# Kernel tuning notes

Hardware: AMD Instinct MI355X
Metric: run time of the kernel (lower is better)

The kernel has to match this reference:

```python
import jax, jax.numpy as jnp
import numpy as np

# Standard SMPL kinematic tree parents (kintree_table)
PARENTS = np.array([-1, 0, 0, 0, 1, 2, 3, 4, 5, 6, 7, 8, 9, 9, 9,
                    12, 13, 14, 16, 17, 18, 19, 20, 21])
NV, NJ, NB, NP = 6890, 24, 10, 207


def rodrigues(r):
    """Axis-angle [N,3] -> rotation matrices [N,3,3] (Rodrigues formula)."""
    theta = jnp.linalg.norm(r, axis=1, keepdims=True) + 1e-8  # [N,1]
    rh = r / theta                                            # [N,3]
    cos = jnp.cos(theta)[..., None]                           # [N,1,1]
    sin = jnp.sin(theta)[..., None]
    z = jnp.zeros_like(rh[:, 0])
    m = jnp.stack([z, -rh[:, 2], rh[:, 1],
                   rh[:, 2], z, -rh[:, 0],
                   -rh[:, 1], rh[:, 0], z], axis=1).reshape(-1, 3, 3)
    dot = rh[:, :, None] * rh[:, None, :]                     # outer product
    eye = jnp.eye(3, dtype=r.dtype)
    return cos * eye + (1.0 - cos) * dot + sin * m


def setup_inputs() -> dict:
    key = jax.random.key(0)
    ks = jax.random.split(key, 9)
    B = 512
    betas = jax.random.normal(ks[0], (B, NB), dtype=jnp.float32)
    thetas = jax.random.normal(ks[1], (B, NJ * 3), dtype=jnp.float32) * 0.3
    trans = jax.random.normal(ks[2], (B, 3), dtype=jnp.float32)
    scale = jnp.ones((1,), dtype=jnp.float32)
    v_template = jax.random.normal(ks[3], (NV, 3), dtype=jnp.float32)
    shapedirs = jax.random.normal(ks[4], (NV, 3, NB), dtype=jnp.float32) * 0.01
    posedirs = jax.random.normal(ks[5], (NV, 3, NP), dtype=jnp.float32) * 0.01
    Jr = jax.random.uniform(ks[6], (NJ, NV), dtype=jnp.float32)
    J_regressor = Jr / jnp.sum(Jr, axis=1, keepdims=True)
    w = jax.random.uniform(ks[7], (NV, NJ), dtype=jnp.float32)
    weights = w / jnp.sum(w, axis=1, keepdims=True)
    return {"betas": betas, "thetas": thetas, "trans": trans, "scale": scale,
            "v_template": v_template, "shapedirs": shapedirs,
            "posedirs": posedirs, "J_regressor": J_regressor,
            "weights": weights}


def reference(betas, thetas, trans, scale, v_template, shapedirs, posedirs,
              J_regressor, weights):
    B = betas.shape[0]
    dt = betas.dtype
    # Shape blend shapes: v_shaped [B, 6890, 3]
    v_shaped = jnp.einsum('bs,vcs->bvc', betas, shapedirs) + v_template
    # Rest-pose joints J(beta): [B, 24, 3]
    J = jnp.einsum('jv,bvc->bjc', J_regressor, v_shaped)
    # Local rotations from axis-angle, root scaled by `scale`
    lRs = rodrigues(thetas.reshape(-1, 3)).reshape(B, NJ, 3, 3)
    lRs = lRs.at[:, 0].multiply(scale[0])
    # Local joint offsets: root keeps J[:,0], children use J[i] - J[parent[i]]
    parents = jnp.asarray(PARENTS)
    t = J - J[:, jnp.clip(parents, 0)]
    t = t.at[:, 0].set(J[:, 0])
    # Local 4x4 transforms [B, 24, 4, 4]
    top = jnp.concatenate([lRs, t[..., None]], axis=3)          # [B,24,3,4]
    bottom = jnp.broadcast_to(jnp.array([0., 0., 0., 1.], dtype=dt),
                              (B, NJ, 1, 4))
    A = jnp.concatenate([top, bottom], axis=2)
    # Kinematic chain accumulation (fixed 24-joint tree)
    results = [A[:, 0]]
    for i in range(1, NJ):
        results.append(results[PARENTS[i]] @ A[:, i])
    stacked = jnp.stack(results, axis=1)                         # [B,24,4,4]
    # Remove rest-pose joint locations from translation column
    Jh = jnp.concatenate([J, jnp.zeros((B, NJ, 1), dtype=dt)], axis=2)
    deformed = jnp.einsum('bjxy,bjy->bjx', stacked, Jh)          # [B,24,4]
    G = stacked.at[..., 3].add(-deformed)
    # Pose blend shapes from non-root rotations
    lrotmin = (lRs[:, 1:] - jnp.eye(3, dtype=dt)).reshape(B, -1)  # [B,207]
    v_posed = v_shaped + jnp.einsum('bp,vcp->bvc', lrotmin, posedirs)
    # Linear blend skinning
    T = jnp.einsum('bjxy,vj->bvxy', G, weights)                  # [B,6890,4,4]
    vh = jnp.concatenate([v_posed, jnp.ones((B, NV, 1), dtype=dt)], axis=2)
    v = jnp.einsum('bvxy,bvy->bvx', T, vh)[:, :, :3]
    result = v + trans[:, None, :]
    joints = jnp.einsum('jv,bvc->bjc', J_regressor, result)
    return result, joints
```

## Files before the change

### kernel.cpp

```cpp
#include <hip/hip_runtime.h>

#define NVERT 6890
#define NJNT  24
#define NBETA 10
#define NPOSE 207
#define NBATCH 512
#define KPAD 224
#define MROWS 20736
#define NVC (NVERT * 3)

#define NBA 18144
#define NBW 1728
#define NJR 576

typedef __attribute__((ext_vector_type(8))) short short8;
typedef __attribute__((ext_vector_type(4))) float floatx4;

__constant__ int c_par[NJNT]   = {-1,0,0,0,1,2,3,4,5,6,7,8,9,9,9,12,13,14,16,17,18,19,20,21};
__constant__ int c_depth[NJNT] = { 0,1,1,1,2,2,2,3,3,3,4,4,4,4,4,5,5,5,6,6,7,7,8,8};

static __device__ __forceinline__ unsigned short f2bf(float x) {
  union { float f; unsigned u; } v; v.f = x;
  unsigned r = (v.u + 0x7FFFu + ((v.u >> 16) & 1u)) >> 16;
  return (unsigned short)r;
}
static __device__ __forceinline__ float bf2f(unsigned short h) {
  union { unsigned u; float f; } v; v.u = (unsigned)h << 16;
  return v.f;
}

__global__ __launch_bounds__(256) void k_prep(
    const float* __restrict__ pdir, const float* __restrict__ sd,
    const float* __restrict__ vt, const float* __restrict__ wgt,
    const float* __restrict__ Jr,
    unsigned short* __restrict__ AT, unsigned short* __restrict__ W16,
    float* __restrict__ wsJP) {
  const int bx = blockIdx.x;
  const int tid = threadIdx.x;
  if (bx < NBA) {
    const int idx = bx * 256 + tid;
    const int kk = idx & 31;
    const int row = (idx >> 5) % MROWS;
    const int kt = idx / (MROWS * 32);
    const int k = kt * 32 + kk;
    float val = 0.f;
    if (row < NVC) {
      if (k < NPOSE)            val = pdir[(size_t)row * NPOSE + k];
      else if (k < NPOSE + 10)  val = sd[(size_t)row * 10 + (k - NPOSE)];
      else if (k == NPOSE + 10) val = vt[row];
    }
    AT[idx] = f2bf(val);
  } else if (bx < NBA + NBW) {
    const int idx = (bx - NBA) * 256 + tid;
    const int v = idx >> 6, c = idx & 63, j = c & 31;
    const float w = (v < NVERT && j < 24) ? wgt[(size_t)v * 24 + j] : 0.f;
    const unsigned short hi = f2bf(w);
    W16[idx] = (c >> 5) ? f2bf(w - bf2f(hi)) : hi;
  } else {
    const int jb = bx - (NBA + NBW);
    const int jc = jb % 72, j = jc / 3, c = jc % 3;
    const int chunk = jb / 72;
    const int v0 = chunk * 864;
    const int vend = min(NVERT, v0 + 864);
    float acc[11];
    #pragma unroll
    for (int k = 0; k < 11; ++k) acc[k] = 0.f;
    for (int v = v0 + tid; v < vend; v += 256) {
      const float w = Jr[j * NVERT + v];
      acc[0] += w * vt[v * 3 + c];
      const float* s = sd + (size_t)v * 30 + c * 10;
      #pragma unroll
      for (int k = 0; k < 10; ++k) acc[1 + k] += w * s[k];
    }
    #pragma unroll
    for (int off = 32; off > 0; off >>= 1) {
      #pragma unroll
      for (int k = 0; k < 11; ++k) acc[k] += __shfl_down(acc[k], off, 64);
    }
    __shared__ float red[4][11];
    const int lane = tid & 63, wv = tid >> 6;
    if (lane == 0) {
      #pragma unroll
      for (int k = 0; k < 11; ++k) red[wv][k] = acc[k];
    }
    __syncthreads();
    if (tid == 0) {
      #pragma unroll
      for (int k = 0; k < 11; ++k)
        wsJP[(size_t)(chunk * 72 + jc) * 11 + k] =
            red[0][k] + red[1][k] + red[2][k] + red[3][k];
    }
  }
}

__global__ __launch_bounds__(256, 2) void k_chain3(
    const float* __restrict__ betas, const float* __restrict__ thetas,
    const float* __restrict__ scale, const float* __restrict__ trans,
    const float* __restrict__ wsJP,
    unsigned short* __restrict__ BT, unsigned short* __restrict__ G16) {
  __shared__ __align__(16) float sJ[792];
  __shared__ __align__(16) float sJJ[4][72];
  __shared__ __align__(16) float sM[4][288];
  __shared__ __align__(16) unsigned short sG[4][1024];
  __shared__ __align__(16) unsigned short sB[4][KPAD];

  const int tid = threadIdx.x;
  const int wv = tid >> 6, lane = tid & 63;
  const int b = blockIdx.x * 4 + wv;

  if (tid < 72) {
    #pragma unroll
    for (int k = 0; k < 11; ++k) {
      float s = 0.f;
      #pragma unroll
      for (int c8 = 0; c8 < 8; ++c8) s += wsJP[(size_t)(c8 * 72 + tid) * 11 + k];
      if (k == 0) sJ[tid] = s;
      else        sJ[72 + tid * 10 + (k - 1)] = s;
    }
  }
  #pragma unroll
  for (int r = 0; r < 4; ++r) {
    sG[wv][lane * 16 + r * 4 + 0] = 0; sG[wv][lane * 16 + r * 4 + 1] = 0;
    sG[wv][lane * 16 + r * 4 + 2] = 0; sG[wv][lane * 16 + r * 4 + 3] = 0;
  }
  __syncthreads();

  float R[9], t[3], M[12], Jx = 0.f, Jy = 0.f, Jz = 0.f;
  const int i = lane;
  if (i < NJNT) {
    #pragma unroll
    for (int c = 0; c < 3; ++c) {
      float a = sJ[i * 3 + c];
      const float* d = sJ + 72 + (i * 3 + c) * 10;
      #pragma unroll
      for (int s = 0; s < NBETA; ++s) a += d[s] * betas[b * NBETA + s];
      if (c == 0) Jx = a; else if (c == 1) Jy = a; else Jz = a;
    }
    sJJ[wv][i * 3 + 0] = Jx; sJJ[wv][i * 3 + 1] = Jy; sJJ[wv][i * 3 + 2] = Jz;
    const float rx = thetas[b * 72 + i * 3 + 0];
    const float ry = thetas[b * 72 + i * 3 + 1];
    const float rz = thetas[b * 72 + i * 3 + 2];
    const float th = sqrtf(rx * rx + ry * ry + rz * rz) + 1e-8f;
    const float inv = 1.f / th;
    const float x = rx * inv, y = ry * inv, z = rz * inv;
    const float cs = cosf(th), sn = sinf(th), omc = 1.f - cs;
    R[0] = cs + omc * x * x;     R[1] = omc * x * y - sn * z; R[2] = omc * x * z + sn * y;
    R[3] = omc * x * y + sn * z; R[4] = cs + omc * y * y;     R[5] = omc * y * z - sn * x;
    R[6] = omc * x * z - sn * y; R[7] = omc * y * z + sn * x; R[8] = cs + omc * z * z;
    if (i == 0) {
      const float sc = scale[0];
      #pragma unroll
      for (int k = 0; k < 9; ++k) R[k] *= sc;
    } else {
      #pragma unroll
      for (int k = 0; k < 9; ++k)
        sB[wv][(i - 1) * 9 + k] = f2bf(R[k] - ((k == 0 || k == 4 || k == 8) ? 1.f : 0.f));
    }
  }
  if (i == 0) {
    #pragma unroll
    for (int s = 0; s < NBETA; ++s) sB[wv][NPOSE + s] = f2bf(betas[b * NBETA + s]);
    sB[wv][NPOSE + 10] = 0x3F80;
    #pragma unroll
    for (int k = NPOSE + 11; k < KPAD; ++k) sB[wv][k] = 0;
  }
  __syncthreads();

  if (i < NJNT) {
    if (i == 0) { t[0] = Jx; t[1] = Jy; t[2] = Jz; }
    else {
      const int p = c_par[i];
      t[0] = Jx - sJJ[wv][p * 3 + 0];
      t[1] = Jy - sJJ[wv][p * 3 + 1];
      t[2] = Jz - sJJ[wv][p * 3 + 2];
    }
    if (i == 0) {
      #pragma unroll
      for (int r = 0; r < 3; ++r) {
        M[r*4+0] = R[r*3+0]; M[r*4+1] = R[r*3+1]; M[r*4+2] = R[r*3+2]; M[r*4+3] = t[r];
      }
      #pragma unroll
      for (int k = 0; k < 12; ++k) sM[wv][k] = M[k];
    }
  }
  __syncthreads();

  for (int lvl = 1; lvl <= 8; ++lvl) {
    if (i < NJNT && c_depth[i] == lvl) {
      const float* Mp = sM[wv] + c_par[i] * 12;
      #pragma unroll
      for (int r = 0; r < 3; ++r) {
        const float p0 = Mp[r*4+0], p1 = Mp[r*4+1], p2 = Mp[r*4+2], p3 = Mp[r*4+3];
        M[r*4+0] = p0*R[0] + p1*R[3] + p2*R[6];
        M[r*4+1] = p0*R[1] + p1*R[4] + p2*R[7];
        M[r*4+2] = p0*R[2] + p1*R[5] + p2*R[8];
        M[r*4+3] = p0*t[0] + p1*t[1] + p2*t[2] + p3;
      }
      #pragma unroll
      for (int k = 0; k < 12; ++k) sM[wv][i * 12 + k] = M[k];
    }
    __syncthreads();
  }

  if (i < NJNT) {
    #pragma unroll
    for (int r = 0; r < 3; ++r) {
      M[r*4+3] = M[r*4+3] - (M[r*4+0]*Jx + M[r*4+1]*Jy + M[r*4+2]*Jz)
               + trans[b * 3 + r];
    }
    #pragma unroll
    for (int e = 0; e < 12; ++e) {
      const float g = M[e];
      const unsigned short hi = f2bf(g);
      sG[wv][e * 32 + i]       = hi;
      sG[wv][512 + e * 32 + i] = f2bf(g - bf2f(hi));
    }
  }
  __syncthreads();

  *(uint4*)(G16 + (size_t)b * 1024 + lane * 16)     = *(uint4*)&sG[wv][lane * 16];
  *(uint4*)(G16 + (size_t)b * 1024 + lane * 16 + 8) = *(uint4*)&sG[wv][lane * 16 + 8];
  if (lane < 28)
    *(uint4*)(BT + ((size_t)(lane >> 2) * NBATCH + b) * 32 + (lane & 3) * 8) =
        *(uint4*)&sB[wv][lane * 8];
}

__global__ __launch_bounds__(256, 3) void k_skin4(
    const unsigned short* __restrict__ AT, const unsigned short* __restrict__ BT,
    const unsigned short* __restrict__ W16, const unsigned short* __restrict__ G16,
    float* __restrict__ out) {
  __shared__ __align__(16) char smem[33536];
  unsigned short* sAs = (unsigned short*)smem;
  unsigned short* sBs = (unsigned short*)(smem + 15360);
  float* sV           = (float*)smem;
  unsigned short* sG2 = (unsigned short*)(smem + 13056);

  const int tid = threadIdx.x;
  const int wv = tid >> 6, lane = tid & 63;
  const int q = lane >> 4, n = lane & 15;

  const int fb = blockIdx.x;
  const int vb = (fb & 7) * 108 + (fb >> 3);
  const int b0 = (vb & 7) * 64;
  const int by = vb >> 3;
  const int vc0 = by * 192;

  floatx4 acc[3][4];
  #pragma unroll
  for (int mt = 0; mt < 3; ++mt)
    #pragma unroll
    for (int nt = 0; nt < 4; ++nt) acc[mt][nt] = (floatx4)(0.f);

  const int srow = tid >> 2, sj = tid & 3;

  uint4 ra[3], rbq;
  #pragma unroll
  for (int it = 0; it < 3; ++it)
    ra[it] = *(const uint4*)(AT + (size_t)(vc0 + it * 64 + srow) * 32 + sj * 8);
  rbq = *(const uint4*)(BT + (size_t)(b0 + srow) * 32 + sj * 8);

  for (int kt = 0; kt < 7; ++kt) {
    if (kt) __syncthreads();
    #pragma unroll
    for (int it = 0; it < 3; ++it)
      *(uint4*)(sAs + (it * 64 + srow) * 40 + sj * 8) = ra[it];
    *(uint4*)(sBs + srow * 40 + sj * 8) = rbq;
    __syncthreads();
    if (kt < 6) {
      #pragma unroll
      for (int it = 0; it < 3; ++it)
        ra[it] = *(const uint4*)(AT +
            ((size_t)(kt + 1) * MROWS + vc0 + it * 64 + srow) * 32 + sj * 8);
      rbq = *(const uint4*)(BT + ((size_t)(kt + 1) * NBATCH + b0 + srow) * 32 + sj * 8);
    }
    short8 af[3], bfr[4];
    #pragma unroll
    for (int mt = 0; mt < 3; ++mt)
      af[mt] = *(const short8*)(sAs + (48 * wv + 16 * mt + n) * 40 + q * 8);
    #pragma unroll
    for (int nt = 0; nt < 4; ++nt)
      bfr[nt] = *(const short8*)(sBs + (16 * nt + n) * 40 + q * 8);
    #pragma unroll
    for (int mt = 0; mt < 3; ++mt)
      #pragma unroll
      for (int nt = 0; nt < 4; ++nt)
        acc[mt][nt] = __builtin_amdgcn_mfma_f32_16x16x32_bf16(
            af[mt], bfr[nt], acc[mt][nt], 0, 0, 0);
  }

  short8 wh[4], wl[4];
  #pragma unroll
  for (int vt = 0; vt < 4; ++vt) {
    const unsigned short* wr = W16 + (size_t)(by * 64 + vt * 16 + n) * 64;
    wh[vt] = *(const short8*)(wr + q * 8);
    wl[vt] = *(const short8*)(wr + 32 + q * 8);
  }

  uint4 gr[4];
  #pragma unroll
  for (int c = 0; c < 4; ++c) {
    const int i = tid + c * 256;
    const int row = i >> 2, c4 = i & 3;
    const int t = row >> 5, rem = row & 31;
    gr[c] = *(const uint4*)(G16 + (size_t)(b0 + t) * 1024 + rem * 32 + c4 * 8);
  }

  for (int nt = 0; nt < 4; ++nt) {
    for (int s = 0; s < 2; ++s) {
      __syncthreads();
      if (s == 0) {
        #pragma unroll
        for (int mt = 0; mt < 3; ++mt)
          #pragma unroll
          for (int r = 0; r < 4; ++r)
            sV[(48 * wv + 16 * mt + 4 * q + r) * 17 + n] = acc[mt][nt][r];
      }
      #pragma unroll
      for (int c = 0; c < 4; ++c) {
        const int i = tid + c * 256;
        const int row = i >> 2, c4 = i & 3;
        *(uint4*)(sG2 + row * 40 + c4 * 8) = gr[c];
      }
      __syncthreads();
      const int rnd = nt * 2 + s;
      if (rnd < 7) {
        const int bg0n = b0 + ((rnd + 1) >> 1) * 16 + ((rnd + 1) & 1) * 8;
        #pragma unroll
        for (int c = 0; c < 4; ++c) {
          const int i = tid + c * 256;
          const int row = i >> 2, c4 = i & 3;
          const int t = row >> 5, rem = row & 31;
          gr[c] = *(const uint4*)(G16 + (size_t)(bg0n + t) * 1024 + rem * 32 + c4 * 8);
        }
      }
      #pragma unroll
      for (int bb = 0; bb < 2; ++bb) {
        const int t = wv * 2 + bb;
        const int col = s * 8 + t;
        const int bg = b0 + nt * 16 + col;
        const short8 gh = *(const short8*)(sG2 + (t * 32 + n) * 40 + q * 8);
        const short8 gl = *(const short8*)(sG2 + (t * 32 + 16 + n) * 40 + q * 8);
        #pragma unroll
        for (int vt = 0; vt < 4; ++vt) {
          floatx4 a2 = (floatx4)(0.f);
          a2 = __builtin_amdgcn_mfma_f32_16x16x32_bf16(gh, wl[vt], a2, 0, 0, 0);
          a2 = __builtin_amdgcn_mfma_f32_16x16x32_bf16(gl, wh[vt], a2, 0, 0, 0);
          a2 = __builtin_amdgcn_mfma_f32_16x16x32_bf16(gh, wh[vt], a2, 0, 0, 0);
          const float X = sV[(48 * vt + 3 * n + 0) * 17 + col];
          const float Y = sV[(48 * vt + 3 * n + 1) * 17 + col];
          const float Z = sV[(48 * vt + 3 * n + 2) * 17 + col];
          const float o = a2[0] * X + a2[1] * Y + a2[2] * Z + a2[3];
          const int vc = vc0 + 48 * vt + 3 * n + q;
          if (q < 3 && vc < NVC)
            out[(size_t)bg * NVC + vc] = o;
        }
      }
    }
  }
}

__global__ __launch_bounds__(256) void k_jnt1(
    const float* __restrict__ Jr, const float* __restrict__ res,
    float* __restrict__ wsJ2) {
  const int b0 = blockIdx.x * 2;
  const int chunk = blockIdx.y;
  const int v0 = chunk * 864;
  const int vend = min(NVERT, v0 + 864);
  const int lane = threadIdx.x & 63, wv = threadIdx.x >> 6;
  float acc[36];
  #pragma unroll
  for (int k = 0; k < 36; ++k) acc[k] = 0.f;
  const float* rA = res + (size_t)b0 * NVC;
  const float* rB = res + (size_t)(b0 + 1) * NVC;
  for (int v = v0 + lane; v < vend; v += 64) {
    const float a0 = rA[v * 3 + 0], a1 = rA[v * 3 + 1], a2 = rA[v * 3 + 2];
    const float e0 = rB[v * 3 + 0], e1 = rB[v * 3 + 1], e2 = rB[v * 3 + 2];
    #pragma unroll
    for (int k = 0; k < 6; ++k) {
      const int j = wv + 4 * k;
      const float w = Jr[j * NVERT + v];
      acc[k*6+0] += w * a0; acc[k*6+1] += w * a1; acc[k*6+2] += w * a2;
      acc[k*6+3] += w * e0; acc[k*6+4] += w * e1; acc[k*6+5] += w * e2;
    }
  }
  #pragma unroll
  for (int off = 32; off > 0; off >>= 1) {
    #pragma unroll
    for (int k = 0; k < 36; ++k) acc[k] += __shfl_down(acc[k], off, 64);
  }
  if (lane == 0) {
    #pragma unroll
    for (int k = 0; k < 6; ++k) {
      const int j = wv + 4 * k;
      float* d0 = wsJ2 + ((size_t)b0 * 8 + chunk) * 72 + j * 3;
      d0[0] = acc[k*6+0]; d0[1] = acc[k*6+1]; d0[2] = acc[k*6+2];
      float* d1 = wsJ2 + ((size_t)(b0 + 1) * 8 + chunk) * 72 + j * 3;
      d1[0] = acc[k*6+3]; d1[1] = acc[k*6+4]; d1[2] = acc[k*6+5];
    }
  }
}

__global__ __launch_bounds__(256) void k_jnt2(
    const float* __restrict__ wsJ2, float* __restrict__ joints) {
  const int idx = blockIdx.x * 256 + threadIdx.x;
  const int b = idx / 72, jc = idx - b * 72;
  float s = 0.f;
  #pragma unroll
  for (int c8 = 0; c8 < 8; ++c8)
    s += wsJ2[((size_t)b * 8 + c8) * 72 + jc];
  joints[idx] = s;
}

extern "C" void kernel_launch(void* const* d_in, const int* in_sizes, int n_in,
                              void* d_out, int out_size, void* d_ws, size_t ws_size,
                              hipStream_t stream) {
  const float* betas  = (const float*)d_in[0];
  const float* thetas = (const float*)d_in[1];
  const float* trans  = (const float*)d_in[2];
  const float* scale  = (const float*)d_in[3];
  const float* vtpl   = (const float*)d_in[4];
  const float* sd     = (const float*)d_in[5];
  const float* pdir   = (const float*)d_in[6];
  const float* Jr     = (const float*)d_in[7];
  const float* wgt    = (const float*)d_in[8];
  float* out = (float*)d_out;

  float* ws   = (float*)d_ws;
  float* wsJP = ws;
  unsigned short* AT  = (unsigned short*)(ws + 6336);
  unsigned short* BT  = AT + (size_t)MROWS * KPAD;
  unsigned short* W16 = BT + (size_t)NBATCH * KPAD;
  unsigned short* G16 = W16 + (size_t)6912 * 64;
  float* wsJ2 = (float*)AT;

  k_prep<<<NBA + NBW + NJR, 256, 0, stream>>>(pdir, sd, vtpl, wgt, Jr, AT, W16, wsJP);
  k_chain3<<<NBATCH / 4, 256, 0, stream>>>(betas, thetas, scale, trans, wsJP, BT, G16);
  k_skin4<<<864, 256, 0, stream>>>(AT, BT, W16, G16, out);
  k_jnt1<<<dim3(NBATCH / 2, 8), 256, 0, stream>>>(Jr, out, wsJ2);
  k_jnt2<<<(NBATCH * 72) / 256, 256, 0, stream>>>(wsJ2, out + (size_t)NBATCH * NVC);
}
```

Measured before the change: 213.6 us.

## Stream GEMM tiles via global_load_lds into double-buffered swizzled LDS

The k-loop of the skinning GEMM now copies A and B tiles straight from global memory into LDS with global_load_lds. It uses two LDS buffers and an XOR-swizzled layout in place of padded rows, so staging through registers and one barrier per iteration go away. Separately, the register prefetch of G tiles in the epilogue is removed and G is loaded synchronously into LDS each round. This lowers register pressure but exposes G load latency in the epilogue. The double buffers (two 16KB regions) overlap the sV and sG2 epilogue regions, which is safe only because of the final barrier in the loop.

```diff
diff --git a/kernel.cpp b/kernel.cpp
--- a/kernel.cpp
+++ b/kernel.cpp
@@ -27,6 +27,12 @@
 static __device__ __forceinline__ float bf2f(unsigned short h) {
   union { unsigned u; float f; } v; v.u = (unsigned)h << 16;
   return v.f;
+}
+
+typedef __attribute__((address_space(1))) const void as1_void;
+typedef __attribute__((address_space(3))) void as3_void;
+static __device__ __forceinline__ void gl_lds16(const void* g, void* l) {
+  __builtin_amdgcn_global_load_lds((as1_void*)g, (as3_void*)l, 16, 0, 0);
 }
 
 __global__ __launch_bounds__(256) void k_prep(
@@ -230,8 +236,6 @@
     const unsigned short* __restrict__ W16, const unsigned short* __restrict__ G16,
     float* __restrict__ out) {
   __shared__ __align__(16) char smem[33536];
-  unsigned short* sAs = (unsigned short*)smem;
-  unsigned short* sBs = (unsigned short*)(smem + 15360);
   float* sV           = (float*)smem;
   unsigned short* sG2 = (unsigned short*)(smem + 13056);
 
@@ -251,41 +255,52 @@
     #pragma unroll
     for (int nt = 0; nt < 4; ++nt) acc[mt][nt] = (floatx4)(0.f);
 
-  const int srow = tid >> 2, sj = tid & 3;
-
-  uint4 ra[3], rbq;
-  #pragma unroll
-  for (int it = 0; it < 3; ++it)
-    ra[it] = *(const uint4*)(AT + (size_t)(vc0 + it * 64 + srow) * 32 + sj * 8);
-  rbq = *(const uint4*)(BT + (size_t)(b0 + srow) * 32 + sj * 8);
-
+  const int stoff = (lane >> 2) * 32 + (((lane & 3) ^ ((lane >> 3) & 3)) * 8);
+  const int rslot = ((lane >> 4) ^ ((lane >> 1) & 3)) * 8;
+
+  const unsigned short* gA0 = AT + ((size_t)vc0 + 48 * wv) * 32 + stoff;
+  const unsigned short* gB0 = BT + ((size_t)b0 + 16 * wv) * 32 + stoff;
+
+  {
+    unsigned short* la = (unsigned short*)smem + 48 * wv * 32;
+    unsigned short* lb = (unsigned short*)(smem + 12288) + 16 * wv * 32;
+    gl_lds16(gA0,        la);
+    gl_lds16(gA0 + 512,  la + 512);
+    gl_lds16(gA0 + 1024, la + 1024);
+    gl_lds16(gB0,        lb);
+  }
+  __syncthreads();
+
+  int cur = 0;
   for (int kt = 0; kt < 7; ++kt) {
-    if (kt) __syncthreads();
-    #pragma unroll
-    for (int it = 0; it < 3; ++it)
-      *(uint4*)(sAs + (it * 64 + srow) * 40 + sj * 8) = ra[it];
-    *(uint4*)(sBs + srow * 40 + sj * 8) = rbq;
-    __syncthreads();
     if (kt < 6) {
-      #pragma unroll
-      for (int it = 0; it < 3; ++it)
-        ra[it] = *(const uint4*)(AT +
-            ((size_t)(kt + 1) * MROWS + vc0 + it * 64 + srow) * 32 + sj * 8);
-      rbq = *(const uint4*)(BT + ((size_t)(kt + 1) * NBATCH + b0 + srow) * 32 + sj * 8);
-    }
+      const int nb = (cur ^ 1) << 14;
+      unsigned short* la = (unsigned short*)(smem + nb) + 48 * wv * 32;
+      unsigned short* lb = (unsigned short*)(smem + nb + 12288) + 16 * wv * 32;
+      const unsigned short* ga = gA0 + (size_t)(kt + 1) * MROWS * 32;
+      const unsigned short* gb = gB0 + (size_t)(kt + 1) * NBATCH * 32;
+      gl_lds16(ga,        la);
+      gl_lds16(ga + 512,  la + 512);
+      gl_lds16(ga + 1024, la + 1024);
+      gl_lds16(gb,        lb);
+    }
+    const unsigned short* sAc = (const unsigned short*)(smem + (cur << 14));
+    const unsigned short* sBc = sAc + 6144;
     short8 af[3], bfr[4];
     #pragma unroll
     for (int mt = 0; mt < 3; ++mt)
-      af[mt] = *(const short8*)(sAs + (48 * wv + 16 * mt + n) * 40 + q * 8);
+      af[mt] = *(const short8*)(sAc + (48 * wv + 16 * mt + n) * 32 + rslot);
     #pragma unroll
     for (int nt = 0; nt < 4; ++nt)
-      bfr[nt] = *(const short8*)(sBs + (16 * nt + n) * 40 + q * 8);
+      bfr[nt] = *(const short8*)(sBc + (16 * nt + n) * 32 + rslot);
     #pragma unroll
     for (int mt = 0; mt < 3; ++mt)
       #pragma unroll
       for (int nt = 0; nt < 4; ++nt)
         acc[mt][nt] = __builtin_amdgcn_mfma_f32_16x16x32_bf16(
             af[mt], bfr[nt], acc[mt][nt], 0, 0, 0);
+    __syncthreads();
+    cur ^= 1;
   }
 
   short8 wh[4], wl[4];
@@ -294,15 +309,6 @@
     const unsigned short* wr = W16 + (size_t)(by * 64 + vt * 16 + n) * 64;
     wh[vt] = *(const short8*)(wr + q * 8);
     wl[vt] = *(const short8*)(wr + 32 + q * 8);
-  }
-
-  uint4 gr[4];
-  #pragma unroll
-  for (int c = 0; c < 4; ++c) {
-    const int i = tid + c * 256;
-    const int row = i >> 2, c4 = i & 3;
-    const int t = row >> 5, rem = row & 31;
-    gr[c] = *(const uint4*)(G16 + (size_t)(b0 + t) * 1024 + rem * 32 + c4 * 8);
   }
 
   for (int nt = 0; nt < 4; ++nt) {
@@ -315,24 +321,14 @@
           for (int r = 0; r < 4; ++r)
             sV[(48 * wv + 16 * mt + 4 * q + r) * 17 + n] = acc[mt][nt][r];
       }
-      #pragma unroll
-      for (int c = 0; c < 4; ++c) {
-        const int i = tid + c * 256;
+      const int bg0 = b0 + nt * 16 + s * 8;
+      for (int i = tid; i < 1024; i += 256) {
         const int row = i >> 2, c4 = i & 3;
-        *(uint4*)(sG2 + row * 40 + c4 * 8) = gr[c];
+        const int t = row >> 5, rem = row & 31;
+        *(uint4*)(sG2 + row * 40 + c4 * 8) =
+            *(const uint4*)(G16 + (size_t)(bg0 + t) * 1024 + rem * 32 + c4 * 8);
       }
       __syncthreads();
-      const int rnd = nt * 2 + s;
-      if (rnd < 7) {
-        const int bg0n = b0 + ((rnd + 1) >> 1) * 16 + ((rnd + 1) & 1) * 8;
-        #pragma unroll
-        for (int c = 0; c < 4; ++c) {
-          const int i = tid + c * 256;
-          const int row = i >> 2, c4 = i & 3;
-          const int t = row >> 5, rem = row & 31;
-          gr[c] = *(const uint4*)(G16 + (size_t)(bg0n + t) * 1024 + rem * 32 + c4 * 8);
-        }
-      }
       #pragma unroll
       for (int bb = 0; bb < 2; ++bb) {
         const int t = wv * 2 + bb;
```

After: 173.9 us. -18.6%, faster.
